# Kernel optimization log

Measured on AMD Instinct MI355X. Metric: run time of the kernel, lower is better.

## Reference

```python
import jax, jax.numpy as jnp
import numpy as np

D_MODEL = 512
NUM_HEADS = 8
D_K = D_MODEL // NUM_HEADS  # 64, also d_v
SEQ_LEN = 4096


def setup_inputs() -> dict:
    key = jax.random.key(0)
    k1, k2, k3, k4, k5 = jax.random.split(key, 5)
    scale = jnp.float32(1.0 / np.sqrt(D_MODEL))  # keep exp(scores) finite
    return {
        "embeded_seq": jax.random.normal(k1, (SEQ_LEN, D_MODEL), jnp.float32),
        "q_proj": jax.random.normal(k2, (NUM_HEADS, D_MODEL, D_K), jnp.float32) * scale,
        "k_proj": jax.random.normal(k3, (NUM_HEADS, D_MODEL, D_K), jnp.float32) * scale,
        "v_proj": jax.random.normal(k4, (NUM_HEADS, D_MODEL, D_K), jnp.float32) * scale,
        "out_proj": jax.random.normal(k5, (NUM_HEADS * D_K, D_MODEL), jnp.float32) * scale,
    }


def reference(embeded_seq, q_proj, k_proj, v_proj, out_proj):
    # Per-head linear projections: (S, D) x (H, D, d_k) -> (H, S, d_k)
    qs = jnp.einsum("sd,hdk->hsk", embeded_seq, q_proj)
    ks = jnp.einsum("sd,hdk->hsk", embeded_seq, k_proj)
    vs = jnp.einsum("sd,hdv->hsv", embeded_seq, v_proj)

    # Scores: (H, S, S), scaled by sqrt(d_k)
    scores = jnp.einsum("hsk,htk->hst", qs, ks) / jnp.float32(np.sqrt(D_K))

    # Faithful to the original: torch.sum(e_powered) is a GLOBAL scalar sum
    # over all heads and positions (a buggy "softmax"), not a row softmax.
    e = jnp.exp(scores)
    softmaxed = e / jnp.sum(e)

    # Attention output per head: (H, S, d_v)
    head_attns = jnp.einsum("hst,htv->hsv", softmaxed, vs)

    # Concat heads along feature dim -> (S, H*d_v), then output projection
    concat = jnp.transpose(head_attns, (1, 0, 2)).reshape(SEQ_LEN, NUM_HEADS * D_K)
    return concat @ out_proj
```

## Files before the change

### kernel.cpp

```cpp
#include <hip/hip_runtime.h>
#include <stdint.h>

#define S_LEN 4096
#define DMODEL 512
#define NHEAD 8
#define DK 64
#define SPLIT 4
#define TBLK 128
#define NT ((S_LEN / SPLIT) / TBLK)

typedef __attribute__((ext_vector_type(8))) short short8;
typedef __attribute__((ext_vector_type(4))) float f32x4;
typedef __attribute__((ext_vector_type(16))) float f32x16;
typedef __attribute__((ext_vector_type(4))) unsigned int uint4v;
typedef __attribute__((ext_vector_type(2))) unsigned long long ull2;

__device__ __forceinline__ unsigned short f2bf(float f) {
    unsigned int u = __float_as_uint(f);
    u = (u + 0x7fffu + ((u >> 16) & 1u)) >> 16;
    return (unsigned short)u;
}

__device__ __forceinline__ void gload16(const unsigned short* g, unsigned short* l) {
    __builtin_amdgcn_global_load_lds(
        (const __attribute__((address_space(1))) unsigned int*)g,
        (__attribute__((address_space(3))) unsigned int*)l, 16, 0, 0);
}


__global__ void cast_bf16_kernel(const float* __restrict__ in,
                                 unsigned short* __restrict__ out, int n4,
                                 float* __restrict__ Z) {
    int i = blockIdx.x * blockDim.x + threadIdx.x;
    if (i == 0) *Z = 0.0f;
    if (i >= n4) return;
    float4 v = reinterpret_cast<const float4*>(in)[i];
    ushort4 o;
    o.x = f2bf(v.x); o.y = f2bf(v.y); o.z = f2bf(v.z); o.w = f2bf(v.w);
    reinterpret_cast<ushort4*>(out)[i] = o;
}

__global__ __launch_bounds__(256) void transpose_qkv_kernel(
    const float* __restrict__ wq, const float* __restrict__ wk, const float* __restrict__ wv,
    unsigned short* __restrict__ oq, unsigned short* __restrict__ ok, unsigned short* __restrict__ ov) {
    __shared__ float tile[64][65];
    const int p = blockIdx.y >> 3, h = blockIdx.y & 7;
    const int r0 = blockIdx.x * 64;
    const float* in = ((p == 0) ? wq : (p == 1) ? wk : wv) + (size_t)h * DMODEL * DK;
    unsigned short* out = ((p == 0) ? oq : (p == 1) ? ok : ov) + (size_t)h * DK * DMODEL;
    const int tr = threadIdx.x >> 4, tc4 = (threadIdx.x & 15) * 4;
#pragma unroll
    for (int rr = 0; rr < 4; ++rr) {
        float4 v = *reinterpret_cast<const float4*>(in + (size_t)(r0 + tr + rr * 16) * DK + tc4);
        tile[tr + rr * 16][tc4 + 0] = v.x;
        tile[tr + rr * 16][tc4 + 1] = v.y;
        tile[tr + rr * 16][tc4 + 2] = v.z;
        tile[tr + rr * 16][tc4 + 3] = v.w;
    }
    __syncthreads();
#pragma unroll
    for (int rr = 0; rr < 4; ++rr) {
        const int c = tr + rr * 16;
        ushort4 o;
        o.x = f2bf(tile[tc4 + 0][c]);
        o.y = f2bf(tile[tc4 + 1][c]);
        o.z = f2bf(tile[tc4 + 2][c]);
        o.w = f2bf(tile[tc4 + 3][c]);
        *reinterpret_cast<ushort4*>(out + (size_t)c * DMODEL + r0 + tc4) = o;
    }
}

__global__ __launch_bounds__(256) void transpose_wo_kernel(
    const float* __restrict__ in, unsigned short* __restrict__ out) {
    __shared__ float tile[64][65];
    const int c0 = blockIdx.x * 64, r0 = blockIdx.y * 64;
    const int tr = threadIdx.x >> 4, tc4 = (threadIdx.x & 15) * 4;
#pragma unroll
    for (int rr = 0; rr < 4; ++rr) {
        float4 v = *reinterpret_cast<const float4*>(in + (size_t)(r0 + tr + rr * 16) * DMODEL + c0 + tc4);
        tile[tr + rr * 16][tc4 + 0] = v.x;
        tile[tr + rr * 16][tc4 + 1] = v.y;
        tile[tr + rr * 16][tc4 + 2] = v.z;
        tile[tr + rr * 16][tc4 + 3] = v.w;
    }
    __syncthreads();
#pragma unroll
    for (int rr = 0; rr < 4; ++rr) {
        const int c = tr + rr * 16;
        ushort4 o;
        o.x = f2bf(tile[tc4 + 0][c]);
        o.y = f2bf(tile[tc4 + 1][c]);
        o.z = f2bf(tile[tc4 + 2][c]);
        o.w = f2bf(tile[tc4 + 3][c]);
        *reinterpret_cast<ushort4*>(out + (size_t)(c0 + c) * DMODEL + r0 + tc4) = o;
    }
}

__global__ __launch_bounds__(256, 2) void proj_tiled_kernel(
    const unsigned short* __restrict__ A,
    const unsigned short* __restrict__ BTall,
    unsigned short* __restrict__ Qo,
    unsigned short* __restrict__ Ko,
    unsigned short* __restrict__ Vo) {
    __shared__ unsigned short lds[32768];
    const int tid = threadIdx.x;
    const int w = tid >> 6, l = tid & 63;
    const int l15 = l & 15, lg = l >> 4;
    const int wr = w >> 1, wc = w & 1;
    const int m0 = blockIdx.x * 128, n0 = blockIdx.y * 128;
    const int srow = l >> 3;
    const int schk = ((l & 7) ^ srow) << 3;
    f32x4 acc[4][4] = {};
    {
        unsigned short* ab = &lds[0];
        unsigned short* bb = &lds[8192];
#pragma unroll
        for (int g = 0; g < 4; ++g) {
            gload16(A + (size_t)(m0 + w * 32 + g * 8 + srow) * DMODEL + schk,
                    ab + (w * 32 + g * 8) * 64);
            gload16(BTall + (size_t)(n0 + w * 32 + g * 8 + srow) * DMODEL + schk,
                    bb + (w * 32 + g * 8) * 64);
        }
    }
    __syncthreads();
    for (int kt = 0; kt < 8; ++kt) {
        const int b = (kt & 1) * 16384;
        if (kt + 1 < 8) {
            const int nb = ((kt + 1) & 1) * 16384;
            const int k0 = (kt + 1) * 64;
            unsigned short* ab = &lds[nb];
            unsigned short* bb = &lds[nb + 8192];
#pragma unroll
            for (int g = 0; g < 4; ++g) {
                gload16(A + (size_t)(m0 + w * 32 + g * 8 + srow) * DMODEL + k0 + schk,
                        ab + (w * 32 + g * 8) * 64);
                gload16(BTall + (size_t)(n0 + w * 32 + g * 8 + srow) * DMODEL + k0 + schk,
                        bb + (w * 32 + g * 8) * 64);
            }
        }
#pragma unroll
        for (int kk = 0; kk < 2; ++kk) {
            short8 am[4], bn[4];
#pragma unroll
            for (int mi = 0; mi < 4; ++mi) {
                const int row = wr * 64 + mi * 16 + l15;
                am[mi] = *reinterpret_cast<const short8*>(
                    &lds[b + row * 64 + ((kk * 32 + lg * 8) ^ ((row & 7) << 3))]);
            }
#pragma unroll
            for (int ni = 0; ni < 4; ++ni) {
                const int row = wc * 64 + ni * 16 + l15;
                bn[ni] = *reinterpret_cast<const short8*>(
                    &lds[b + 8192 + row * 64 + ((kk * 32 + lg * 8) ^ ((row & 7) << 3))]);
            }
#pragma unroll
            for (int mi = 0; mi < 4; ++mi)
#pragma unroll
                for (int ni = 0; ni < 4; ++ni)
                    acc[mi][ni] = __builtin_amdgcn_mfma_f32_16x16x32_bf16(am[mi], bn[ni], acc[mi][ni], 0, 0, 0);
        }
        __syncthreads();
    }
#pragma unroll
    for (int ni = 0; ni < 4; ++ni) {
        const int n = n0 + wc * 64 + ni * 16;
        const int p = n >> 9, h = (n >> 6) & 7, vb = n & 63;
        unsigned short* dst = ((p == 0) ? Qo : (p == 1) ? Ko : Vo) + (size_t)h * S_LEN * DK;
        const float sc = (p == 0) ? 0.125f : 1.0f;
#pragma unroll
        for (int mi = 0; mi < 4; ++mi) {
            const int s = m0 + wr * 64 + mi * 16 + lg * 4;
#pragma unroll
            for (int r = 0; r < 4; ++r)
                dst[(size_t)(s + r) * DK + vb + l15] = f2bf(acc[mi][ni][r] * sc);
        }
    }
}

__global__ __launch_bounds__(256, 2) void out_tiled_kernel(
    const unsigned short* __restrict__ A,
    const unsigned short* __restrict__ BT,
    const float* __restrict__ Z,
    float* __restrict__ Cout) {
    __shared__ unsigned short lds[32768];
    const int tid = threadIdx.x;
    const int w = tid >> 6, l = tid & 63;
    const int l15 = l & 15, lg = l >> 4;
    const int wr = w >> 1, wc = w & 1;
    const int m0 = blockIdx.x * 128, n0 = blockIdx.y * 128;
    const int srow = l >> 3;
    const int schk = ((l & 7) ^ srow) << 3;
    const float invZ = 1.0f / *Z;
    f32x4 acc[4][4] = {};
    {
        unsigned short* ab = &lds[0];
        unsigned short* bb = &lds[8192];
#pragma unroll
        for (int g = 0; g < 4; ++g) {
            gload16(A + (size_t)(m0 + w * 32 + g * 8 + srow) * DMODEL + schk,
                    ab + (w * 32 + g * 8) * 64);
            gload16(BT + (size_t)(n0 + w * 32 + g * 8 + srow) * DMODEL + schk,
                    bb + (w * 32 + g * 8) * 64);
        }
    }
    __syncthreads();
    for (int kt = 0; kt < 8; ++kt) {
        const int b = (kt & 1) * 16384;
        if (kt + 1 < 8) {
            const int nb = ((kt + 1) & 1) * 16384;
            const int k0 = (kt + 1) * 64;
            unsigned short* ab = &lds[nb];
            unsigned short* bb = &lds[nb + 8192];
#pragma unroll
            for (int g = 0; g < 4; ++g) {
                gload16(A + (size_t)(m0 + w * 32 + g * 8 + srow) * DMODEL + k0 + schk,
                        ab + (w * 32 + g * 8) * 64);
                gload16(BT + (size_t)(n0 + w * 32 + g * 8 + srow) * DMODEL + k0 + schk,
                        bb + (w * 32 + g * 8) * 64);
            }
        }
#pragma unroll
        for (int kk = 0; kk < 2; ++kk) {
            short8 am[4], bn[4];
#pragma unroll
            for (int mi = 0; mi < 4; ++mi) {
                const int row = wr * 64 + mi * 16 + l15;
                am[mi] = *reinterpret_cast<const short8*>(
                    &lds[b + row * 64 + ((kk * 32 + lg * 8) ^ ((row & 7) << 3))]);
            }
#pragma unroll
            for (int ni = 0; ni < 4; ++ni) {
                const int row = wc * 64 + ni * 16 + l15;
                bn[ni] = *reinterpret_cast<const short8*>(
                    &lds[b + 8192 + row * 64 + ((kk * 32 + lg * 8) ^ ((row & 7) << 3))]);
            }
#pragma unroll
            for (int mi = 0; mi < 4; ++mi)
#pragma unroll
                for (int ni = 0; ni < 4; ++ni)
                    acc[mi][ni] = __builtin_amdgcn_mfma_f32_16x16x32_bf16(am[mi], bn[ni], acc[mi][ni], 0, 0, 0);
        }
        __syncthreads();
    }
#pragma unroll
    for (int ni = 0; ni < 4; ++ni) {
        const int n = n0 + wc * 64 + ni * 16;
#pragma unroll
        for (int mi = 0; mi < 4; ++mi) {
            const int s = m0 + wr * 64 + mi * 16 + lg * 4;
#pragma unroll
            for (int r = 0; r < 4; ++r)
                Cout[(size_t)(s + r) * DMODEL + n + l15] = acc[mi][ni][r] * invZ;
        }
    }
}

__global__ __launch_bounds__(256) void vt_kernel(const unsigned short* __restrict__ Vb,
                                                 unsigned short* __restrict__ VT) {
    __shared__ unsigned short tile[4096];
    int h = blockIdx.y, t0 = blockIdx.x * 64;
    const unsigned short* Vh = Vb + h * (S_LEN * DK);
    unsigned short* VTh = VT + h * (DK * S_LEN);
    int c8 = (threadIdx.x & 7) * 8, rw = threadIdx.x >> 3;
#pragma unroll
    for (int rr = 0; rr < 2; ++rr) {
        int t = rw + rr * 32;
        short8 v = *reinterpret_cast<const short8*>(Vh + (t0 + t) * DK + c8);
        *reinterpret_cast<short8*>(&tile[t * 64 + (c8 ^ ((t & 7) << 3))]) = v;
    }
    __syncthreads();
#pragma unroll
    for (int rr = 0; rr < 2; ++rr) {
        int v = rw + rr * 32;
        short8 s;
#pragma unroll
        for (int i = 0; i < 8; ++i) {
            int t = c8 + i;
            s[i] = (short)tile[t * 64 + (v ^ ((t & 7) << 3))];
        }
        *reinterpret_cast<short8*>(VTh + v * S_LEN + t0 + c8) = s;
    }
}

__device__ __forceinline__ void make_pfrag(const f32x16& s, short8 pf[2],
                                           float& z0, float& z1) {
    float p[16];
#pragma unroll
    for (int r = 0; r < 16; ++r) p[r] = __expf(s[r]);
#pragma unroll
    for (int r = 0; r < 16; r += 2) { z0 += p[r]; z1 += p[r + 1]; }
    unsigned int c[8];
#pragma unroll
    for (int j = 0; j < 8; ++j)
        asm("v_cvt_pk_bf16_f32 %0, %1, %2" : "=v"(c[j]) : "v"(p[2 * j]), "v"(p[2 * j + 1]));
    uint4v wa = {c[0], c[1], c[2], c[3]};
    uint4v wb = {c[4], c[5], c[6], c[7]};
    pf[0] = __builtin_bit_cast(short8, wa);
    pf[1] = __builtin_bit_cast(short8, wb);
}

__global__ __launch_bounds__(256, 2) void attn_kernel(
    const unsigned short* __restrict__ Qg,
    const unsigned short* __restrict__ Kg,
    const unsigned short* __restrict__ VTg,
    float* __restrict__ Opart,
    float* __restrict__ Z) {
    __shared__ unsigned short lds[32768];
    const int tid = threadIdx.x;
    const int w = tid >> 6, l = tid & 63;
    const int l31 = l & 31, lh = l >> 5;
    const int qb = blockIdx.x, h = blockIdx.y, sp = blockIdx.z;
    const unsigned short* Qh = Qg + h * (S_LEN * DK);
    const unsigned short* Kh = Kg + h * (S_LEN * DK);
    const unsigned short* VTh = VTg + h * (DK * S_LEN);
    const int t_base = sp * (S_LEN / SPLIT);
    const int q0 = qb * 256 + w * 64;

    short8 bq[2][4];
#pragma unroll
    for (int qc = 0; qc < 2; ++qc)
#pragma unroll
        for (int ks = 0; ks < 4; ++ks)
            bq[qc][ks] = *reinterpret_cast<const short8*>(
                Qh + (q0 + qc * 32 + l31) * DK + ks * 16 + lh * 8);

    f32x16 oacc[2][2] = {};
    float z0 = 0.0f, z1 = 0.0f;

    const int kr = l >> 3;
    const int kc = (((l & 7) ^ kr) << 3);
    const int vr = l >> 4;

    {
        unsigned short* kb = &lds[0];
        unsigned short* vbuf = &lds[8192];
#pragma unroll
        for (int g = 0; g < 4; ++g) {
            gload16(Kh + (size_t)(t_base + w * 32 + g * 8 + kr) * DK + kc,
                    kb + (w * 32 + g * 8) * 64);
            const int row = w * 16 + g * 4 + vr;
            const int chk = ((l & 15) ^ (row & 7)) << 3;
            gload16(VTh + (size_t)row * S_LEN + t_base + chk,
                    vbuf + (w * 16 + g * 4) * 128);
        }
    }
    __syncthreads();

    for (int it = 0; it < NT; ++it) {
        const int b = (it & 1) * 16384;
        if (it + 1 < NT) {
            const int nbuf = ((it + 1) & 1) * 16384;
            const int t0 = t_base + (it + 1) * TBLK;
            unsigned short* kb = &lds[nbuf];
            unsigned short* vbuf = &lds[nbuf + 8192];
#pragma unroll
            for (int g = 0; g < 4; ++g) {
                gload16(Kh + (size_t)(t0 + w * 32 + g * 8 + kr) * DK + kc,
                        kb + (w * 32 + g * 8) * 64);
                const int row = w * 16 + g * 4 + vr;
                const int chk = ((l & 15) ^ (row & 7)) << 3;
                gload16(VTh + (size_t)row * S_LEN + t0 + chk,
                        vbuf + (w * 16 + g * 4) * 128);
            }
        }
#pragma unroll
        for (int tc = 0; tc < 4; ++tc) {
            f32x16 s0 = {}, s1 = {};
            const int tA = tc * 32 + l31;
#pragma unroll
            for (int ks = 0; ks < 4; ++ks) {
                short8 ka = *reinterpret_cast<const short8*>(
                    &lds[b + tA * 64 + ((ks * 16 + lh * 8) ^ ((tA & 7) << 3))]);
                s0 = __builtin_amdgcn_mfma_f32_32x32x16_bf16(ka, bq[0][ks], s0, 0, 0, 0);
                s1 = __builtin_amdgcn_mfma_f32_32x32x16_bf16(ka, bq[1][ks], s1, 0, 0, 0);
            }
            short8 pf0[2], pf1[2];
            make_pfrag(s0, pf0, z0, z1);
            make_pfrag(s1, pf1, z0, z1);
#pragma unroll
            for (int sub = 0; sub < 2; ++sub) {
#pragma unroll
                for (int vc = 0; vc < 2; ++vc) {
                    const int vx = l31 & 7;
                    const int cc = tc * 4 + sub * 2;
                    const int base = b + 16384 - 8192 + (vc * 32 + l31) * 128;
                    unsigned long long d0 = *reinterpret_cast<const unsigned long long*>(
                        &lds[b + 8192 + (vc * 32 + l31) * 128 + ((cc ^ vx) << 3) + lh * 4]);
                    unsigned long long d1 = *reinterpret_cast<const unsigned long long*>(
                        &lds[b + 8192 + (vc * 32 + l31) * 128 + (((cc + 1) ^ vx) << 3) + lh * 4]);
                    (void)base;
                    ull2 dd = {d0, d1};
                    short8 bv = __builtin_bit_cast(short8, dd);
                    oacc[0][vc] = __builtin_amdgcn_mfma_f32_32x32x16_bf16(pf0[sub], bv, oacc[0][vc], 0, 0, 0);
                    oacc[1][vc] = __builtin_amdgcn_mfma_f32_32x32x16_bf16(pf1[sub], bv, oacc[1][vc], 0, 0, 0);
                }
            }
        }
        __syncthreads();
    }
    float* Op = Opart + ((size_t)(sp * NHEAD + h) * S_LEN + q0) * DK;
#pragma unroll
    for (int qc = 0; qc < 2; ++qc)
#pragma unroll
        for (int vc = 0; vc < 2; ++vc)
#pragma unroll
            for (int reg = 0; reg < 16; ++reg) {
                int q = qc * 32 + (reg & 3) + 8 * (reg >> 2) + 4 * lh;
                Op[(size_t)q * DK + vc * 32 + l31] = oacc[qc][vc][reg];
            }
    float zloc = z0 + z1;
#pragma unroll
    for (int off = 32; off > 0; off >>= 1) zloc += __shfl_xor(zloc, off, 64);
    if (l == 0) atomicAdd(Z, zloc);
}

__global__ __launch_bounds__(256) void reduce_o_kernel(
    const float* __restrict__ Opart, unsigned short* __restrict__ cc) {
    const int HSV = NHEAD * S_LEN * DK;
    int i = blockIdx.x * blockDim.x + threadIdx.x;
    if (i * 4 >= HSV) return;
    f32x4 s = {};
#pragma unroll
    for (int sp = 0; sp < SPLIT; ++sp) {
        f32x4 v = *reinterpret_cast<const f32x4*>(&Opart[(size_t)sp * HSV + i * 4]);
        s += v;
    }
    int e = i * 4;
    int h = e / (S_LEN * DK);
    int rem = e - h * (S_LEN * DK);
    int srow = rem / DK;
    int v = rem - srow * DK;
    ushort4 o4;
    o4.x = f2bf(s[0]); o4.y = f2bf(s[1]); o4.z = f2bf(s[2]); o4.w = f2bf(s[3]);
    *reinterpret_cast<ushort4*>(&cc[srow * DMODEL + h * DK + v]) = o4;
}


extern "C" void kernel_launch(void* const* d_in, const int* in_sizes, int n_in,
                              void* d_out, int out_size, void* d_ws, size_t ws_size,
                              hipStream_t stream) {
    const float* emb = (const float*)d_in[0];
    const float* wq = (const float*)d_in[1];
    const float* wk = (const float*)d_in[2];
    const float* wv = (const float*)d_in[3];
    const float* wo = (const float*)d_in[4];
    float* out = (float*)d_out;
    char* ws = (char*)d_ws;
    unsigned short* embB = (unsigned short*)(ws);
    unsigned short* wqT  = (unsigned short*)(ws + 4194304);
    unsigned short* wkT  = (unsigned short*)(ws + 4718592);
    unsigned short* wvT  = (unsigned short*)(ws + 5242880);
    unsigned short* woT  = (unsigned short*)(ws + 5767168);
    unsigned short* Qb   = (unsigned short*)(ws + 6291456);
    unsigned short* Kb   = (unsigned short*)(ws + 10485760);
    unsigned short* Vb   = (unsigned short*)(ws + 14680064);
    unsigned short* cc   = (unsigned short*)(ws + 18874368);
    float* Z             = (float*)(ws + 23068672);
    float* Opart         = (float*)(ws + 23072768);
    unsigned short* VT   = embB;

    cast_bf16_kernel<<<2048, 256, 0, stream>>>(emb, embB, 524288, Z);
    transpose_qkv_kernel<<<dim3(8, 24), 256, 0, stream>>>(wq, wk, wv, wqT, wkT, wvT);
    transpose_wo_kernel<<<dim3(8, 8), 256, 0, stream>>>(wo, woT);
    proj_tiled_kernel<<<dim3(32, 12), 256, 0, stream>>>(embB, wqT, Qb, Kb, Vb);
    vt_kernel<<<dim3(64, 8), 256, 0, stream>>>(Vb, VT);
    attn_kernel<<<dim3(16, 8, SPLIT), 256, 0, stream>>>(Qb, Kb, VT, Opart, Z);
    reduce_o_kernel<<<2048, 256, 0, stream>>>(Opart, cc);
    out_tiled_kernel<<<dim3(32, 4), 256, 0, stream>>>(cc, woT, Z, out);
}
```

Baseline: 103.0 us.

## Use 4-stage LDS ring with prefetch depth two and finer vmcnt waits

Shrinks the key/value tile from 128 to 64 keys and replaces the double-buffered loads with a four-slot LDS ring that prefetches two tiles ahead. Each iteration waits only for the tile it needs via explicit s_waitcnt vmcnt counts and a single raw barrier, instead of a full __syncthreads after each tile. It also raises wave priority around the MFMA sections. The aim is to hide global load latency better and cut barrier stalls, at the cost of more iterations and fragile hand-counted wait values that depend on how the compiler orders the loads.

```diff
diff --git a/kernel.cpp b/kernel.cpp
--- a/kernel.cpp
+++ b/kernel.cpp
@@ -6,7 +6,7 @@
 #define NHEAD 8
 #define DK 64
 #define SPLIT 4
-#define TBLK 128
+#define TBLK 64
 #define NT ((S_LEN / SPLIT) / TBLK)
 
 typedef __attribute__((ext_vector_type(8))) short short8;
@@ -327,46 +327,35 @@
     f32x16 oacc[2][2] = {};
     float z0 = 0.0f, z1 = 0.0f;
 
-    const int kr = l >> 3;
-    const int kc = (((l & 7) ^ kr) << 3);
-    const int vr = l >> 4;
-
-    {
-        unsigned short* kb = &lds[0];
-        unsigned short* vbuf = &lds[8192];
-#pragma unroll
-        for (int g = 0; g < 4; ++g) {
-            gload16(Kh + (size_t)(t_base + w * 32 + g * 8 + kr) * DK + kc,
-                    kb + (w * 32 + g * 8) * 64);
-            const int row = w * 16 + g * 4 + vr;
-            const int chk = ((l & 15) ^ (row & 7)) << 3;
-            gload16(VTh + (size_t)row * S_LEN + t_base + chk,
-                    vbuf + (w * 16 + g * 4) * 128);
-        }
-    }
-    __syncthreads();
-
+    const int srow = l >> 3;
+    const int scol = ((l & 7) ^ srow) << 3;
+    const unsigned short* gkb = Kh + (size_t)(t_base + w * 16 + srow) * DK + scol;
+    const unsigned short* gvb = VTh + (size_t)(w * 16 + srow) * S_LEN + t_base + scol;
+
+    auto stage = [&](int tt) {
+        const int boff = (tt & 3) * 8192;
+        unsigned short* kb = &lds[boff + w * 1024];
+        unsigned short* vb = &lds[boff + 4096 + w * 1024];
+        gload16(gkb + (size_t)tt * TBLK * DK, kb);
+        gload16(gkb + (size_t)tt * TBLK * DK + 8 * DK, kb + 512);
+        gload16(gvb + tt * TBLK, vb);
+        gload16(gvb + tt * TBLK + 8 * S_LEN, vb + 512);
+    };
+
+    stage(0);
+    stage(1);
     for (int it = 0; it < NT; ++it) {
-        const int b = (it & 1) * 16384;
-        if (it + 1 < NT) {
-            const int nbuf = ((it + 1) & 1) * 16384;
-            const int t0 = t_base + (it + 1) * TBLK;
-            unsigned short* kb = &lds[nbuf];
-            unsigned short* vbuf = &lds[nbuf + 8192];
-#pragma unroll
-            for (int g = 0; g < 4; ++g) {
-                gload16(Kh + (size_t)(t0 + w * 32 + g * 8 + kr) * DK + kc,
-                        kb + (w * 32 + g * 8) * 64);
-                const int row = w * 16 + g * 4 + vr;
-                const int chk = ((l & 15) ^ (row & 7)) << 3;
-                gload16(VTh + (size_t)row * S_LEN + t0 + chk,
-                        vbuf + (w * 16 + g * 4) * 128);
-            }
-        }
-#pragma unroll
-        for (int tc = 0; tc < 4; ++tc) {
+        if (it + 2 < NT) stage(it + 2);
+        if (it < NT - 2)       asm volatile("s_waitcnt vmcnt(8)" ::: "memory");
+        else if (it == NT - 2) asm volatile("s_waitcnt vmcnt(4)" ::: "memory");
+        else                   asm volatile("s_waitcnt vmcnt(0)" ::: "memory");
+        __builtin_amdgcn_s_barrier();
+        const int b = (it & 3) * 8192;
+#pragma unroll
+        for (int tc = 0; tc < 2; ++tc) {
             f32x16 s0 = {}, s1 = {};
             const int tA = tc * 32 + l31;
+            __builtin_amdgcn_s_setprio(1);
 #pragma unroll
             for (int ks = 0; ks < 4; ++ks) {
                 short8 ka = *reinterpret_cast<const short8*>(
@@ -374,29 +363,30 @@
                 s0 = __builtin_amdgcn_mfma_f32_32x32x16_bf16(ka, bq[0][ks], s0, 0, 0, 0);
                 s1 = __builtin_amdgcn_mfma_f32_32x32x16_bf16(ka, bq[1][ks], s1, 0, 0, 0);
             }
+            __builtin_amdgcn_s_setprio(0);
             short8 pf0[2], pf1[2];
             make_pfrag(s0, pf0, z0, z1);
             make_pfrag(s1, pf1, z0, z1);
+            __builtin_amdgcn_s_setprio(1);
 #pragma unroll
             for (int sub = 0; sub < 2; ++sub) {
 #pragma unroll
                 for (int vc = 0; vc < 2; ++vc) {
                     const int vx = l31 & 7;
                     const int cc = tc * 4 + sub * 2;
-                    const int base = b + 16384 - 8192 + (vc * 32 + l31) * 128;
+                    const int base = b + 4096 + (vc * 32 + l31) * 64;
                     unsigned long long d0 = *reinterpret_cast<const unsigned long long*>(
-                        &lds[b + 8192 + (vc * 32 + l31) * 128 + ((cc ^ vx) << 3) + lh * 4]);
+                        &lds[base + ((cc ^ vx) << 3) + lh * 4]);
                     unsigned long long d1 = *reinterpret_cast<const unsigned long long*>(
-                        &lds[b + 8192 + (vc * 32 + l31) * 128 + (((cc + 1) ^ vx) << 3) + lh * 4]);
-                    (void)base;
+                        &lds[base + (((cc + 1) ^ vx) << 3) + lh * 4]);
                     ull2 dd = {d0, d1};
                     short8 bv = __builtin_bit_cast(short8, dd);
                     oacc[0][vc] = __builtin_amdgcn_mfma_f32_32x32x16_bf16(pf0[sub], bv, oacc[0][vc], 0, 0, 0);
                     oacc[1][vc] = __builtin_amdgcn_mfma_f32_32x32x16_bf16(pf1[sub], bv, oacc[1][vc], 0, 0, 0);
                 }
             }
-        }
-        __syncthreads();
+            __builtin_amdgcn_s_setprio(0);
+        }
     }
     float* Op = Opart + ((size_t)(sp * NHEAD + h) * S_LEN + q0) * DK;
 #pragma unroll
```

Measured after the change: 105.9 us. 2.8% more time.
